# Kernel tuning notes

Hardware: AMD Instinct MI355X
Metric: run time of the kernel (lower is better)

## Reference

```python
import jax, jax.numpy as jnp
import numpy as np

NEG_SLOPE = 0.2
EPS = 1e-16


def setup_inputs() -> dict:
    N, E, IN, H, C = 100000, 1600000, 128, 4, 16
    key = jax.random.key(0)
    k1, k2, k3, k4, k5 = jax.random.split(key, 5)
    x = jax.random.normal(k1, (N, IN), dtype=jnp.float32)
    edge_index = jax.random.randint(k2, (2, E), 0, N, dtype=jnp.int64)
    # Xavier-uniform init like nn.init.xavier_uniform_
    limW = float(np.sqrt(6.0 / (IN + H * C)))
    W = jax.random.uniform(k3, (IN, H * C), dtype=jnp.float32, minval=-limW, maxval=limW)
    lima = float(np.sqrt(6.0 / (H + C)))
    att = jax.random.uniform(k4, (1, H, C), dtype=jnp.float32, minval=-lima, maxval=lima)
    bias = jnp.zeros((H * C,), dtype=jnp.float32)
    return {"x": x, "edge_index": edge_index, "W": W, "att": att, "bias": bias}


def reference(x, edge_index, W, att, bias):
    N = x.shape[0]
    H, C = att.shape[1], att.shape[2]
    h = (x @ W).reshape(N, H, C)  # [N,H,C]
    # add self loops
    loops = jnp.arange(N, dtype=edge_index.dtype)
    row = jnp.concatenate([edge_index[0], loops])  # target nodes
    col = jnp.concatenate([edge_index[1], loops])  # source nodes
    x_i = h[row]  # [Etot,H,C]
    x_j = h[col]
    e = jax.nn.leaky_relu(x_i + x_j, NEG_SLOPE)
    alpha = jnp.einsum('ehc,hc->eh', e, att[0])  # [Etot,H]
    # segment softmax keyed by row (every node has a self loop -> no empty segments)
    amax = jax.lax.stop_gradient(jax.ops.segment_max(alpha, row, num_segments=N))
    ea = jnp.exp(alpha - amax[row])
    denom = jax.ops.segment_sum(ea, row, num_segments=N)
    alpha = ea / (denom[row] + EPS)
    # weighted message scatter-add (dropout p=0 / eval mode)
    out = jax.ops.segment_sum(x_j * alpha[:, :, None], row, num_segments=N)  # [N,H,C]
    out = out.reshape(N, H * C) + bias  # concat=True
    return out
```

## Files before the change

### kernel.cpp

```cpp
#include <hip/hip_runtime.h>

#define NEG_SLOPE 0.2f

typedef float f32x4 __attribute__((ext_vector_type(4)));
typedef short bf16x8 __attribute__((ext_vector_type(8)));

__device__ __forceinline__ unsigned short f2bf(float f) {
  union { float f; unsigned u; } v; v.f = f;
  unsigned r = v.u + 0x7fff + ((v.u >> 16) & 1);
  return (unsigned short)(r >> 16);
}
__device__ __forceinline__ float bf2f(unsigned short u) {
  union { unsigned u; float f; } v; v.u = ((unsigned)u) << 16;
  return v.f;
}
__device__ __forceinline__ unsigned pkbf(float a, float b) {
  return (unsigned)f2bf(a) | ((unsigned)f2bf(b) << 16);
}
__device__ __forceinline__ f32x4 upk4(unsigned ux, unsigned uy) {
  union { unsigned u; float f; } a, b, c, d;
  a.u = ux << 16; b.u = ux & 0xffff0000u;
  c.u = uy << 16; d.u = uy & 0xffff0000u;
  f32x4 r; r.x = a.f; r.y = b.f; r.z = c.f; r.w = d.f;
  return r;
}
__device__ __forceinline__ f32x4 absfma(f32x4 s, f32x4 coef, f32x4 d) {
  d.x = fmaf(fabsf(s.x), coef.x, d.x);
  d.y = fmaf(fabsf(s.y), coef.y, d.y);
  d.z = fmaf(fabsf(s.z), coef.z, d.z);
  d.w = fmaf(fabsf(s.w), coef.w, d.w);
  return d;
}
__device__ __forceinline__ float dpp_xor1_add(float x) {
  int y = __builtin_amdgcn_mov_dpp(__builtin_bit_cast(int, x), 0xB1, 0xF, 0xF, true);
  return x + __builtin_bit_cast(float, y);
}
__device__ __forceinline__ float dpp_xor2_add(float x) {
  int y = __builtin_amdgcn_mov_dpp(__builtin_bit_cast(int, x), 0x4E, 0xF, 0xF, true);
  return x + __builtin_bit_cast(float, y);
}

#define TILE 4096
#define EPT 16
#define NBKT_MAX 256
#define SMEM_BYTES 24576

__device__ __forceinline__ void gemm_role(const float* __restrict__ x,
                                          const float* __restrict__ W,
                                          unsigned short* __restrict__ hb, int N,
                                          char* smem, int bid) {
  uint4* Bl = (uint4*)smem;
  const int t = threadIdx.x;
  {
    const int l = t & 63;
    const int kt = (t >> 6) & 3;
    const int kb = kt * 32 + ((l >> 4) * 8);
    const int cb = l & 15;
#pragma unroll
    for (int ct = 0; ct < 4; ct++) {
      const float* wp = W + (size_t)kb * 64 + ct * 16 + cb;
      unsigned p[4];
#pragma unroll
      for (int jj = 0; jj < 4; jj++)
        p[jj] = pkbf(wp[(2 * jj) * 64], wp[(2 * jj + 1) * 64]);
      Bl[(ct * 4 + kt) * 64 + l] = make_uint4(p[0], p[1], p[2], p[3]);
    }
  }
  __syncthreads();
  const int l = t & 63;
  const int wv = t >> 6;
  union BU { bf16x8 v; uint4 q; };
  BU b[4][4];
#pragma unroll
  for (int ct = 0; ct < 4; ct++)
#pragma unroll
    for (int kt = 0; kt < 4; kt++) b[ct][kt].q = Bl[(ct * 4 + kt) * 64 + l];

  const int rowbase0 = bid * 256 + wv * 64;
#pragma unroll
  for (int rt = 0; rt < 4; rt++) {
    const int rbase = rowbase0 + rt * 16;
    int rl = rbase + (l & 15);
    if (rl >= N) rl = N - 1;
    const float* xp = x + (size_t)rl * 128 + ((l >> 4) * 8);
    BU ah[4], alo[4];
#pragma unroll
    for (int kt = 0; kt < 4; kt++) {
      float f[8];
      float4 v0 = *(const float4*)(xp + kt * 32);
      float4 v1 = *(const float4*)(xp + kt * 32 + 4);
      f[0] = v0.x; f[1] = v0.y; f[2] = v0.z; f[3] = v0.w;
      f[4] = v1.x; f[5] = v1.y; f[6] = v1.z; f[7] = v1.w;
      unsigned short hs[8], ls[8];
#pragma unroll
      for (int j = 0; j < 8; j++) {
        hs[j] = f2bf(f[j]);
        ls[j] = f2bf(f[j] - bf2f(hs[j]));
      }
      ah[kt].q = make_uint4(hs[0] | (hs[1] << 16), hs[2] | (hs[3] << 16),
                            hs[4] | (hs[5] << 16), hs[6] | (hs[7] << 16));
      alo[kt].q = make_uint4(ls[0] | (ls[1] << 16), ls[2] | (ls[3] << 16),
                             ls[4] | (ls[5] << 16), ls[6] | (ls[7] << 16));
    }
#pragma unroll
    for (int ct = 0; ct < 4; ct++) {
      f32x4 acc = {0.f, 0.f, 0.f, 0.f};
#pragma unroll
      for (int kt = 0; kt < 4; kt++) {
        acc = __builtin_amdgcn_mfma_f32_16x16x32_bf16(ah[kt].v, b[ct][kt].v, acc, 0, 0, 0);
        acc = __builtin_amdgcn_mfma_f32_16x16x32_bf16(alo[kt].v, b[ct][kt].v, acc, 0, 0, 0);
      }
#pragma unroll
      for (int j = 0; j < 4; j++) {
        float v = acc[j];
        float pv = __shfl_xor(v, 1);
        int row = rbase + (l >> 4) * 4 + j;
        if (!(l & 1) && row < N) {
          *(unsigned*)((char*)hb + (size_t)row * 128 + ct * 32 + (l & 15) * 2) =
              pkbf(v, pv);
        }
      }
    }
  }
}

__device__ __forceinline__ void bucket_role(const int* __restrict__ rowi,
                                            const int* __restrict__ coli,
                                            int* __restrict__ bucket_fill,
                                            unsigned* __restrict__ bucket_arr, int E,
                                            int Cedge, int Ctot, int NBKT, char* smem,
                                            int bid) {
  int* cnt = (int*)smem;
  int* gadj = cnt + 256;
  int* tmp = gadj + 256;
  unsigned* staged = (unsigned*)(tmp + 256);
  unsigned char* bkof = (unsigned char*)(staged + TILE);
  const int t = threadIdx.x;
  const int tile0 = bid * TILE;
  const int nt = min(TILE, E - tile0);
  cnt[t] = 0;
  __syncthreads();
  unsigned pk[EPT];
  int bk[EPT];
#pragma unroll
  for (int j = 0; j < EPT; j++) {
    int i = tile0 + j * 256 + t;
    if (i < E) {
      int r = rowi[i];
      int c = coli[i];
      bk[j] = r >> 9;
      pk[j] = ((unsigned)(r & 511) << 17) | (unsigned)c;
      atomicAdd(&cnt[bk[j]], 1);
    } else {
      bk[j] = -1;
    }
  }
  __syncthreads();
  int v = cnt[t];
  tmp[t] = v;
  __syncthreads();
  for (int off = 1; off < 256; off <<= 1) {
    int val = tmp[t] + ((t >= off) ? tmp[t - off] : 0);
    __syncthreads();
    tmp[t] = val;
    __syncthreads();
  }
  int ex = tmp[t] - v;
  int ga = 0;
  if (v > 0) ga = atomicAdd(&bucket_fill[t], v);
  gadj[t] = ga - ex;
  cnt[t] = ex;
  __syncthreads();
#pragma unroll
  for (int j = 0; j < EPT; j++) {
    if (bk[j] >= 0) {
      int lp = atomicAdd(&cnt[bk[j]], 1);
      staged[lp] = pk[j];
      bkof[lp] = (unsigned char)bk[j];
    }
  }
  __syncthreads();
  for (int i = t; i < nt; i += 256) {
    int b = bkof[i];
    int pb = i + gadj[b];
    if (pb < Cedge) bucket_arr[b * Ctot + pb] = staged[i];
  }
}

__global__ __launch_bounds__(256) void gemm_bucket(const float* __restrict__ x,
                                                   const float* __restrict__ W,
                                                   unsigned short* __restrict__ hb, int N,
                                                   const int* __restrict__ rowi,
                                                   const int* __restrict__ coli,
                                                   int* __restrict__ bucket_fill,
                                                   unsigned* __restrict__ bucket_arr,
                                                   int E, int Cedge, int Ctot, int NBKT,
                                                   int G1) {
  __shared__ __align__(16) char smem[SMEM_BYTES];
  if ((int)blockIdx.x < G1)
    gemm_role(x, W, hb, N, smem, blockIdx.x);
  else
    bucket_role(rowi, coli, bucket_fill, bucket_arr, E, Cedge, Ctot, NBKT, smem,
                blockIdx.x - G1);
}

#define STAGE_CAP 10240

__global__ __launch_bounds__(1024) void csr_pass(unsigned* __restrict__ bucket_arr,
                                                 const int* __restrict__ bucket_fill,
                                                 int2* __restrict__ rowinfo,
                                                 int Cedge, int Ctot, int N) {
  __shared__ unsigned stage[STAGE_CAP];
  __shared__ int hist[512], excl[512], pairs[256];
  const int t = threadIdx.x;
  const int b = blockIdx.x;
  const int bb = b * Ctot;
  const int r0 = b << 9;
  const int nb = min(bucket_fill[b], Cedge);
  for (int i = t; i < 512; i += 1024) hist[i] = ((r0 + i) < N) ? 1 : 0;
  for (int i = t; i < nb; i += 1024) stage[i] = bucket_arr[bb + i];
  __syncthreads();
  for (int i = t; i < nb; i += 1024) atomicAdd(&hist[stage[i] >> 17], 1);
  __syncthreads();
  int h0 = 0, h1 = 0, ps = 0;
  if (t < 256) {
    h0 = hist[2 * t];
    h1 = hist[2 * t + 1];
    ps = h0 + h1;
    pairs[t] = ps;
  }
  __syncthreads();
  for (int off = 1; off < 256; off <<= 1) {
    int val = 0;
    if (t < 256) val = pairs[t] + ((t >= off) ? pairs[t - off] : 0);
    __syncthreads();
    if (t < 256) pairs[t] = val;
    __syncthreads();
  }
  if (t < 256) {
    int pexcl = pairs[t] - ps;
    excl[2 * t] = pexcl;
    excl[2 * t + 1] = pexcl + h0;
  }
  __syncthreads();
  for (int r = t; r < 512; r += 1024) {
    int gr = r0 + r;
    if (gr < N) {
      int o = bb + excl[r];
      rowinfo[gr] = make_int2(o, o + hist[r]);
    }
  }
  __syncthreads();
  for (int i = t; i < nb; i += 1024) {
    unsigned pk = stage[i];
    int r = pk >> 17;
    int lp = atomicAdd(&excl[r], 1);
    bucket_arr[bb + lp] = (pk & 0x1FFFFu) << 7;
  }
  __syncthreads();
  for (int r = t; r < 512; r += 1024) {
    int gr = r0 + r;
    if (gr < N) bucket_arr[bb + excl[r]] = (unsigned)gr << 7;
  }
}

#define ESTEPN(hivX, accX, denX, u)                     \
  {                                                     \
    f32x4 jv = upk4((u).x, (u).y);                      \
    f32x4 s = hivX + jv;                                \
    f32x4 d = s * attA;                                 \
    d = absfma(s, attB, d);                             \
    float al = (d.x + d.y) + (d.z + d.w);               \
    al = dpp_xor1_add(al);                              \
    al = dpp_xor2_add(al);                              \
    float p = __expf(al);                               \
    accX += jv * p;                                     \
    denX += p;                                          \
  }

__global__ __launch_bounds__(256) void node_pass(const unsigned short* __restrict__ hb,
                                                 const int2* __restrict__ rowinfo,
                                                 const unsigned* __restrict__ srcs,
                                                 const float* __restrict__ att,
                                                 const float* __restrict__ bias,
                                                 float* __restrict__ out, int N) {
  const int wp = (blockIdx.x * blockDim.x + threadIdx.x) >> 6;
  const int a = wp * 2;
  if (a >= N) return;
  const int bn = a + 1;
  const bool bvalid = bn < N;
  const int bc = bvalid ? bn : a;
  const int lane = threadIdx.x & 63;
  const int lr = lane & 15;
  const int q = lane >> 4;
  const char* hbc = (const char*)hb;
  const unsigned loff = (unsigned)(lr << 3);
  const f32x4 attv = *(const f32x4*)(att + 4 * lr);
  const f32x4 attA = attv * 0.6f;
  const f32x4 attB = attv * 0.4f;
  const int2 ria = rowinfo[a];
  const int2 rib = rowinfo[bc];
  uint2 hua = *(const uint2*)(hbc + (((unsigned)a << 7) | loff));
  uint2 hub = *(const uint2*)(hbc + (((unsigned)bc << 7) | loff));
  const f32x4 hivA = upk4(hua.x, hua.y);
  const f32x4 hivB = upk4(hub.x, hub.y);
  int ka = ria.x, kb = rib.x;
  const int ka1 = ria.y;
  const int kb1 = bvalid ? rib.y : rib.x;
  f32x4 accA = {0.f, 0.f, 0.f, 0.f};
  f32x4 accB = {0.f, 0.f, 0.f, 0.f};
  float denA = 0.f, denB = 0.f;
  while (ka + 8 <= ka1 && kb + 8 <= kb1) {
    unsigned oa0 = srcs[ka + q] | loff;
    unsigned oa1 = srcs[ka + 4 + q] | loff;
    unsigned ob0 = srcs[kb + q] | loff;
    unsigned ob1 = srcs[kb + 4 + q] | loff;
    uint2 ua0 = *(const uint2*)(hbc + oa0);
    uint2 ua1 = *(const uint2*)(hbc + oa1);
    uint2 ub0 = *(const uint2*)(hbc + ob0);
    uint2 ub1 = *(const uint2*)(hbc + ob1);
    ESTEPN(hivA, accA, denA, ua0);
    ESTEPN(hivA, accA, denA, ua1);
    ESTEPN(hivB, accB, denB, ub0);
    ESTEPN(hivB, accB, denB, ub1);
    ka += 8;
    kb += 8;
  }
  for (; ka + 8 <= ka1; ka += 8) {
    unsigned o0 = srcs[ka + q] | loff;
    unsigned o1 = srcs[ka + 4 + q] | loff;
    uint2 u0 = *(const uint2*)(hbc + o0);
    uint2 u1 = *(const uint2*)(hbc + o1);
    ESTEPN(hivA, accA, denA, u0);
    ESTEPN(hivA, accA, denA, u1);
  }
  for (; kb + 8 <= kb1; kb += 8) {
    unsigned o0 = srcs[kb + q] | loff;
    unsigned o1 = srcs[kb + 4 + q] | loff;
    uint2 u0 = *(const uint2*)(hbc + o0);
    uint2 u1 = *(const uint2*)(hbc + o1);
    ESTEPN(hivB, accB, denB, u0);
    ESTEPN(hivB, accB, denB, u1);
  }
  for (; ka + 4 <= ka1; ka += 4) {
    unsigned o = srcs[ka + q] | loff;
    uint2 u = *(const uint2*)(hbc + o);
    ESTEPN(hivA, accA, denA, u);
  }
  for (; kb + 4 <= kb1; kb += 4) {
    unsigned o = srcs[kb + q] | loff;
    uint2 u = *(const uint2*)(hbc + o);
    ESTEPN(hivB, accB, denB, u);
  }
  if (ka < ka1) {
    bool act = (ka + q) < ka1;
    unsigned o = (act ? srcs[ka + q] : srcs[ka]) | loff;
    uint2 u = *(const uint2*)(hbc + o);
    f32x4 jv = upk4(u.x, u.y);
    f32x4 s = hivA + jv;
    f32x4 d = s * attA;
    d = absfma(s, attB, d);
    float al = (d.x + d.y) + (d.z + d.w);
    al = dpp_xor1_add(al);
    al = dpp_xor2_add(al);
    float p = act ? __expf(al) : 0.f;
    accA += jv * p;
    denA += p;
  }
  if (kb < kb1) {
    bool act = (kb + q) < kb1;
    unsigned o = (act ? srcs[kb + q] : srcs[kb]) | loff;
    uint2 u = *(const uint2*)(hbc + o);
    f32x4 jv = upk4(u.x, u.y);
    f32x4 s = hivB + jv;
    f32x4 d = s * attA;
    d = absfma(s, attB, d);
    float al = (d.x + d.y) + (d.z + d.w);
    al = dpp_xor1_add(al);
    al = dpp_xor2_add(al);
    float p = act ? __expf(al) : 0.f;
    accB += jv * p;
    denB += p;
  }
#pragma unroll
  for (int j = 0; j < 4; j++) {
    accA[j] += __shfl_xor(accA[j], 16);
    accB[j] += __shfl_xor(accB[j], 16);
    accA[j] += __shfl_xor(accA[j], 32);
    accB[j] += __shfl_xor(accB[j], 32);
  }
  denA += __shfl_xor(denA, 16);
  denB += __shfl_xor(denB, 16);
  denA += __shfl_xor(denA, 32);
  denB += __shfl_xor(denB, 32);
  if (q == 0) {
    const f32x4 bv = *(const f32x4*)(bias + 4 * lr);
    float invA = 1.0f / (denA + 1e-16f);
    f32x4 oa = accA * invA + bv;
    *(f32x4*)(out + (size_t)a * 64 + 4 * lr) = oa;
    if (bvalid) {
      float invB = 1.0f / (denB + 1e-16f);
      f32x4 ob = accB * invB + bv;
      *(f32x4*)(out + (size_t)bn * 64 + 4 * lr) = ob;
    }
  }
}

extern "C" void kernel_launch(void* const* d_in, const int* in_sizes, int n_in,
                              void* d_out, int out_size, void* d_ws, size_t ws_size,
                              hipStream_t stream) {
  const float* x = (const float*)d_in[0];
  const int* eidx = (const int*)d_in[1];
  const float* W = (const float*)d_in[2];
  const float* att = (const float*)d_in[3];
  const float* bias = (const float*)d_in[4];
  float* out = (float*)d_out;

  const int N = in_sizes[0] / 128;
  const int E = in_sizes[1] / 2;
  const int NBKT = (N + 511) >> 9;
  int Cedge = (E + NBKT - 1) / NBKT;
  Cedge = Cedge + Cedge / 8 + 64;
  Cedge = (Cedge + 15) & ~15;
  if (Cedge > STAGE_CAP) Cedge = STAGE_CAP;
  const int Ctot = Cedge + 512;

  unsigned short* hb = (unsigned short*)d_ws;
  int* bucket_fill = (int*)(hb + (size_t)N * 64);
  int2* rowinfo = (int2*)(bucket_fill + NBKT_MAX);
  unsigned* bucket_arr = (unsigned*)(rowinfo + N);

  hipMemsetAsync(bucket_fill, 0, NBKT_MAX * sizeof(int), stream);

  const int G1 = (N + 255) / 256;
  const int G2 = (E + TILE - 1) / TILE;
  gemm_bucket<<<G1 + G2, 256, 0, stream>>>(x, W, hb, N, eidx, eidx + E, bucket_fill,
                                           bucket_arr, E, Cedge, Ctot, NBKT, G1);
  csr_pass<<<NBKT, 1024, 0, stream>>>(bucket_arr, bucket_fill, rowinfo, Cedge, Ctot, N);
  const int npairs = (N + 1) / 2;
  node_pass<<<(npairs * 64 + 255) / 256, 256, 0, stream>>>(hb, rowinfo, bucket_arr, att,
                                                           bias, out, N);
}
```

Before: 101.0 us.

## Make node_pass persistent with prefetch of next pair, exp2 with folded log2e

The node aggregation kernel becomes a grid-stride persistent kernel on a fixed grid of 2048 blocks. Each wave prefetches the rowinfo and self-features of its next node pair while it processes the current one. The attention coefficients are pre-scaled by log2(e) so the exponential becomes exp2f. Source offset addressing is simplified by folding the lane offset into the base pointer, and launch bounds now request occupancy. The aim is to hide per-pair startup latency and trim ALU work, at the cost of a fixed grid size that may under- or over-subscribe the device.

```diff
diff --git a/kernel.cpp b/kernel.cpp
--- a/kernel.cpp
+++ b/kernel.cpp
@@ -273,136 +273,150 @@
     float al = (d.x + d.y) + (d.z + d.w);               \
     al = dpp_xor1_add(al);                              \
     al = dpp_xor2_add(al);                              \
-    float p = __expf(al);                               \
+    float p = exp2f(al);                                \
     accX += jv * p;                                     \
     denX += p;                                          \
   }
 
-__global__ __launch_bounds__(256) void node_pass(const unsigned short* __restrict__ hb,
-                                                 const int2* __restrict__ rowinfo,
-                                                 const unsigned* __restrict__ srcs,
-                                                 const float* __restrict__ att,
-                                                 const float* __restrict__ bias,
-                                                 float* __restrict__ out, int N) {
-  const int wp = (blockIdx.x * blockDim.x + threadIdx.x) >> 6;
-  const int a = wp * 2;
-  if (a >= N) return;
-  const int bn = a + 1;
-  const bool bvalid = bn < N;
-  const int bc = bvalid ? bn : a;
+__global__ __launch_bounds__(256, 7) void node_pass(const unsigned short* __restrict__ hb,
+                                                    const int2* __restrict__ rowinfo,
+                                                    const unsigned* __restrict__ srcs,
+                                                    const float* __restrict__ att,
+                                                    const float* __restrict__ bias,
+                                                    float* __restrict__ out, int N) {
+  const int gw = (blockIdx.x * blockDim.x + threadIdx.x) >> 6;
+  const int nw = (gridDim.x * blockDim.x) >> 6;
   const int lane = threadIdx.x & 63;
   const int lr = lane & 15;
   const int q = lane >> 4;
-  const char* hbc = (const char*)hb;
-  const unsigned loff = (unsigned)(lr << 3);
+  const char* hbc = (const char*)hb + (unsigned)(lr << 3);
+  const unsigned* srcq = srcs + q;
   const f32x4 attv = *(const f32x4*)(att + 4 * lr);
-  const f32x4 attA = attv * 0.6f;
-  const f32x4 attB = attv * 0.4f;
-  const int2 ria = rowinfo[a];
-  const int2 rib = rowinfo[bc];
-  uint2 hua = *(const uint2*)(hbc + (((unsigned)a << 7) | loff));
-  uint2 hub = *(const uint2*)(hbc + (((unsigned)bc << 7) | loff));
-  const f32x4 hivA = upk4(hua.x, hua.y);
-  const f32x4 hivB = upk4(hub.x, hub.y);
-  int ka = ria.x, kb = rib.x;
-  const int ka1 = ria.y;
-  const int kb1 = bvalid ? rib.y : rib.x;
-  f32x4 accA = {0.f, 0.f, 0.f, 0.f};
-  f32x4 accB = {0.f, 0.f, 0.f, 0.f};
-  float denA = 0.f, denB = 0.f;
-  while (ka + 8 <= ka1 && kb + 8 <= kb1) {
-    unsigned oa0 = srcs[ka + q] | loff;
-    unsigned oa1 = srcs[ka + 4 + q] | loff;
-    unsigned ob0 = srcs[kb + q] | loff;
-    unsigned ob1 = srcs[kb + 4 + q] | loff;
-    uint2 ua0 = *(const uint2*)(hbc + oa0);
-    uint2 ua1 = *(const uint2*)(hbc + oa1);
-    uint2 ub0 = *(const uint2*)(hbc + ob0);
-    uint2 ub1 = *(const uint2*)(hbc + ob1);
-    ESTEPN(hivA, accA, denA, ua0);
-    ESTEPN(hivA, accA, denA, ua1);
-    ESTEPN(hivB, accB, denB, ub0);
-    ESTEPN(hivB, accB, denB, ub1);
-    ka += 8;
-    kb += 8;
-  }
-  for (; ka + 8 <= ka1; ka += 8) {
-    unsigned o0 = srcs[ka + q] | loff;
-    unsigned o1 = srcs[ka + 4 + q] | loff;
-    uint2 u0 = *(const uint2*)(hbc + o0);
-    uint2 u1 = *(const uint2*)(hbc + o1);
-    ESTEPN(hivA, accA, denA, u0);
-    ESTEPN(hivA, accA, denA, u1);
-  }
-  for (; kb + 8 <= kb1; kb += 8) {
-    unsigned o0 = srcs[kb + q] | loff;
-    unsigned o1 = srcs[kb + 4 + q] | loff;
-    uint2 u0 = *(const uint2*)(hbc + o0);
-    uint2 u1 = *(const uint2*)(hbc + o1);
-    ESTEPN(hivB, accB, denB, u0);
-    ESTEPN(hivB, accB, denB, u1);
-  }
-  for (; ka + 4 <= ka1; ka += 4) {
-    unsigned o = srcs[ka + q] | loff;
-    uint2 u = *(const uint2*)(hbc + o);
-    ESTEPN(hivA, accA, denA, u);
-  }
-  for (; kb + 4 <= kb1; kb += 4) {
-    unsigned o = srcs[kb + q] | loff;
-    uint2 u = *(const uint2*)(hbc + o);
-    ESTEPN(hivB, accB, denB, u);
-  }
-  if (ka < ka1) {
-    bool act = (ka + q) < ka1;
-    unsigned o = (act ? srcs[ka + q] : srcs[ka]) | loff;
-    uint2 u = *(const uint2*)(hbc + o);
-    f32x4 jv = upk4(u.x, u.y);
-    f32x4 s = hivA + jv;
-    f32x4 d = s * attA;
-    d = absfma(s, attB, d);
-    float al = (d.x + d.y) + (d.z + d.w);
-    al = dpp_xor1_add(al);
-    al = dpp_xor2_add(al);
-    float p = act ? __expf(al) : 0.f;
-    accA += jv * p;
-    denA += p;
-  }
-  if (kb < kb1) {
-    bool act = (kb + q) < kb1;
-    unsigned o = (act ? srcs[kb + q] : srcs[kb]) | loff;
-    uint2 u = *(const uint2*)(hbc + o);
-    f32x4 jv = upk4(u.x, u.y);
-    f32x4 s = hivB + jv;
-    f32x4 d = s * attA;
-    d = absfma(s, attB, d);
-    float al = (d.x + d.y) + (d.z + d.w);
-    al = dpp_xor1_add(al);
-    al = dpp_xor2_add(al);
-    float p = act ? __expf(al) : 0.f;
-    accB += jv * p;
-    denB += p;
-  }
-#pragma unroll
-  for (int j = 0; j < 4; j++) {
-    accA[j] += __shfl_xor(accA[j], 16);
-    accB[j] += __shfl_xor(accB[j], 16);
-    accA[j] += __shfl_xor(accA[j], 32);
-    accB[j] += __shfl_xor(accB[j], 32);
-  }
-  denA += __shfl_xor(denA, 16);
-  denB += __shfl_xor(denB, 16);
-  denA += __shfl_xor(denA, 32);
-  denB += __shfl_xor(denB, 32);
-  if (q == 0) {
-    const f32x4 bv = *(const f32x4*)(bias + 4 * lr);
-    float invA = 1.0f / (denA + 1e-16f);
-    f32x4 oa = accA * invA + bv;
-    *(f32x4*)(out + (size_t)a * 64 + 4 * lr) = oa;
-    if (bvalid) {
-      float invB = 1.0f / (denB + 1e-16f);
-      f32x4 ob = accB * invB + bv;
-      *(f32x4*)(out + (size_t)bn * 64 + 4 * lr) = ob;
-    }
+  const f32x4 attA = attv * (0.6f * 1.44269504088896f);
+  const f32x4 attB = attv * (0.4f * 1.44269504088896f);
+  const int npair = (N + 1) >> 1;
+  int wp = gw;
+  if (wp >= npair) return;
+  int a0 = wp << 1;
+  bool bval = a0 + 1 < N;
+  int bc = bval ? a0 + 1 : a0;
+  int2 ria = rowinfo[a0];
+  int2 rib = rowinfo[bc];
+  uint2 hua = *(const uint2*)(hbc + ((size_t)a0 << 7));
+  uint2 hub = *(const uint2*)(hbc + ((size_t)bc << 7));
+  for (;;) {
+    const int wpn = wp + nw;
+    const bool more = wpn < npair;
+    int an = 0, bcn = 0;
+    bool bvn = false;
+    int2 rian = ria, ribn = rib;
+    uint2 huan = hua, hubn = hub;
+    if (more) {
+      an = wpn << 1;
+      bvn = an + 1 < N;
+      bcn = bvn ? an + 1 : an;
+      rian = rowinfo[an];
+      ribn = rowinfo[bcn];
+      huan = *(const uint2*)(hbc + ((size_t)an << 7));
+      hubn = *(const uint2*)(hbc + ((size_t)bcn << 7));
+    }
+    const f32x4 hivA = upk4(hua.x, hua.y);
+    const f32x4 hivB = upk4(hub.x, hub.y);
+    int ka = ria.x, kb = rib.x;
+    const int ka1 = ria.y;
+    const int kb1 = bval ? rib.y : rib.x;
+    f32x4 accA = {0.f, 0.f, 0.f, 0.f};
+    f32x4 accB = {0.f, 0.f, 0.f, 0.f};
+    float denA = 0.f, denB = 0.f;
+    while (ka + 8 <= ka1 && kb + 8 <= kb1) {
+      uint2 ua0 = *(const uint2*)(hbc + srcq[ka]);
+      uint2 ua1 = *(const uint2*)(hbc + srcq[ka + 4]);
+      uint2 ub0 = *(const uint2*)(hbc + srcq[kb]);
+      uint2 ub1 = *(const uint2*)(hbc + srcq[kb + 4]);
+      ESTEPN(hivA, accA, denA, ua0);
+      ESTEPN(hivA, accA, denA, ua1);
+      ESTEPN(hivB, accB, denB, ub0);
+      ESTEPN(hivB, accB, denB, ub1);
+      ka += 8;
+      kb += 8;
+    }
+    for (; ka + 8 <= ka1; ka += 8) {
+      uint2 u0 = *(const uint2*)(hbc + srcq[ka]);
+      uint2 u1 = *(const uint2*)(hbc + srcq[ka + 4]);
+      ESTEPN(hivA, accA, denA, u0);
+      ESTEPN(hivA, accA, denA, u1);
+    }
+    for (; kb + 8 <= kb1; kb += 8) {
+      uint2 u0 = *(const uint2*)(hbc + srcq[kb]);
+      uint2 u1 = *(const uint2*)(hbc + srcq[kb + 4]);
+      ESTEPN(hivB, accB, denB, u0);
+      ESTEPN(hivB, accB, denB, u1);
+    }
+    for (; ka + 4 <= ka1; ka += 4) {
+      uint2 u = *(const uint2*)(hbc + srcq[ka]);
+      ESTEPN(hivA, accA, denA, u);
+    }
+    for (; kb + 4 <= kb1; kb += 4) {
+      uint2 u = *(const uint2*)(hbc + srcq[kb]);
+      ESTEPN(hivB, accB, denB, u);
+    }
+    if (ka < ka1) {
+      bool act = (ka + q) < ka1;
+      uint2 u = *(const uint2*)(hbc + (act ? srcq[ka] : srcs[ka]));
+      f32x4 jv = upk4(u.x, u.y);
+      f32x4 s = hivA + jv;
+      f32x4 d = s * attA;
+      d = absfma(s, attB, d);
+      float al = (d.x + d.y) + (d.z + d.w);
+      al = dpp_xor1_add(al);
+      al = dpp_xor2_add(al);
+      float p = act ? exp2f(al) : 0.f;
+      accA += jv * p;
+      denA += p;
+    }
+    if (kb < kb1) {
+      bool act = (kb + q) < kb1;
+      uint2 u = *(const uint2*)(hbc + (act ? srcq[kb] : srcs[kb]));
+      f32x4 jv = upk4(u.x, u.y);
+      f32x4 s = hivB + jv;
+      f32x4 d = s * attA;
+      d = absfma(s, attB, d);
+      float al = (d.x + d.y) + (d.z + d.w);
+      al = dpp_xor1_add(al);
+      al = dpp_xor2_add(al);
+      float p = act ? exp2f(al) : 0.f;
+      accB += jv * p;
+      denB += p;
+    }
+#pragma unroll
+    for (int j = 0; j < 4; j++) {
+      accA[j] += __shfl_xor(accA[j], 16);
+      accB[j] += __shfl_xor(accB[j], 16);
+      accA[j] += __shfl_xor(accA[j], 32);
+      accB[j] += __shfl_xor(accB[j], 32);
+    }
+    denA += __shfl_xor(denA, 16);
+    denB += __shfl_xor(denB, 16);
+    denA += __shfl_xor(denA, 32);
+    denB += __shfl_xor(denB, 32);
+    if (q == 0) {
+      const f32x4 bv = *(const f32x4*)(bias + 4 * lr);
+      float invA = 1.0f / (denA + 1e-16f);
+      *(f32x4*)(out + (size_t)a0 * 64 + 4 * lr) = accA * invA + bv;
+      if (bval) {
+        float invB = 1.0f / (denB + 1e-16f);
+        *(f32x4*)(out + (size_t)(a0 + 1) * 64 + 4 * lr) = accB * invB + bv;
+      }
+    }
+    if (!more) break;
+    wp = wpn;
+    a0 = an;
+    bval = bvn;
+    bc = bcn;
+    ria = rian;
+    rib = ribn;
+    hua = huan;
+    hub = hubn;
   }
 }
 
@@ -437,7 +451,5 @@
   gemm_bucket<<<G1 + G2, 256, 0, stream>>>(x, W, hb, N, eidx, eidx + E, bucket_fill,
                                            bucket_arr, E, Cedge, Ctot, NBKT, G1);
   csr_pass<<<NBKT, 1024, 0, stream>>>(bucket_arr, bucket_fill, rowinfo, Cedge, Ctot, N);
-  const int npairs = (N + 1) / 2;
-  node_pass<<<(npairs * 64 + 255) / 256, 256, 0, stream>>>(hb, rowinfo, bucket_arr, att,
-                                                           bias, out, N);
-}
+  node_pass<<<2048, 256, 0, stream>>>(hb, rowinfo, bucket_arr, att, bias, out, N);
+}
```

Result: slower. 132.0 us (+30.6%).
